# Kernel tuning notes

Hardware: AMD Instinct MI355X
Metric: run time of the kernel (lower is better)

Reference implementation:

```python
import jax, jax.numpy as jnp
import numpy as np

N_NODES = 200000
N_EDGES = 6400000
N_GRAPHS = 2000


def _linear_params(key, fan_in, fan_out):
    k1, k2 = jax.random.split(key)
    bound = 1.0 / np.sqrt(fan_in)
    W = jax.random.uniform(k1, (fan_in, fan_out), minval=-bound, maxval=bound, dtype=jnp.float32)
    b = jax.random.uniform(k2, (fan_out,), minval=-bound, maxval=bound, dtype=jnp.float32)
    return W, b


def setup_inputs() -> dict:
    key = jax.random.key(0)
    ks = jax.random.split(key, 12)
    x = jax.random.normal(ks[0], (N_NODES, 2), dtype=jnp.float32)
    edge_index = jax.random.randint(ks[1], (2, N_EDGES), 0, N_NODES, dtype=jnp.int32)
    batch = jnp.sort(jax.random.randint(ks[2], (N_NODES,), 0, N_GRAPHS, dtype=jnp.int32))
    W1a, b1a = _linear_params(ks[3], 2, 16)
    W1b, b1b = _linear_params(ks[4], 16, 16)
    W2a, b2a = _linear_params(ks[5], 16, 16)
    W2b, b2b = _linear_params(ks[6], 16, 16)
    W3a, b3a = _linear_params(ks[7], 16, 16)
    W3b, b3b = _linear_params(ks[8], 16, 16)
    Wl1, bl1 = _linear_params(ks[9], 16, 16)
    Wl2, bl2 = _linear_params(ks[10], 16, 1)
    return dict(x=x, edge_index=edge_index, batch=batch,
                W1a=W1a, b1a=b1a, W1b=W1b, b1b=b1b,
                W2a=W2a, b2a=b2a, W2b=W2b, b2b=b2b,
                W3a=W3a, b3a=b3a, W3b=W3b, b3b=b3b,
                Wl1=Wl1, bl1=bl1, Wl2=Wl2, bl2=bl2)


def _gin_conv(x, src, dst, Wa, ba, Wb, bb):
    # sum-aggregate neighbor features at destination nodes; eps = 0
    msgs = x[src]                                            # [E, d]
    aggr = jax.ops.segment_sum(msgs, dst, num_segments=N_NODES)  # [N, d]
    h = x + aggr
    h = jax.nn.relu(h @ Wa + ba)
    return h @ Wb + bb


def reference(x, edge_index, batch,
              W1a, b1a, W1b, b1b,
              W2a, b2a, W2b, b2b,
              W3a, b3a, W3b, b3b,
              Wl1, bl1, Wl2, bl2):
    src, dst = edge_index[0], edge_index[1]
    h = jax.nn.relu(_gin_conv(x, src, dst, W1a, b1a, W1b, b1b))
    h = jax.nn.relu(_gin_conv(h, src, dst, W2a, b2a, W2b, b2b))
    h = jax.nn.relu(_gin_conv(h, src, dst, W3a, b3a, W3b, b3b))
    g = jax.ops.segment_sum(h, batch, num_segments=N_GRAPHS)  # global_add_pool -> [G, 16]
    g = jax.nn.relu(g @ Wl1 + bl1)
    return g @ Wl2 + bl2                                      # [G, 1]
```

## Files before the change

### kernel.cpp

```cpp
#include <hip/hip_runtime.h>

#define N_NODES 200000
#define N_EDGES 6400000
#define N_GRAPHS 2000

#define MBSHIFT 11
#define NMB 98
#define MBCAP 67584
#define CHUNK 8192
#define PBLK 782
#define PB 9

#define FSHIFT 7
#define NBUCK 1563
#define CAPF 4608

__device__ __forceinline__ float bf_lo(unsigned v) { return __uint_as_float(v << 16); }
__device__ __forceinline__ float bf_hi(unsigned v) { return __uint_as_float(v & 0xFFFF0000u); }
__device__ __forceinline__ unsigned pack_bf2(float lo, float hi) {
  unsigned a = __float_as_uint(lo), b = __float_as_uint(hi);
  a = (a + 0x7FFFu + ((a >> 16) & 1u)) >> 16;
  b = (b + 0x7FFFu + ((b >> 16) & 1u)) >> 16;
  return a | (b << 16);
}

__global__ __launch_bounds__(256) void init_cursors(int* __restrict__ gcurA,
                                                    int* __restrict__ gcur2) {
  int i = blockIdx.x * 256 + threadIdx.x;
  if (i < NMB) gcurA[i] = i * MBCAP;
  if (i < NMB * 16) gcur2[i] = i * CAPF;
}

__global__ __launch_bounds__(256) void partA(
    const int* __restrict__ src, const int* __restrict__ dst,
    int* __restrict__ gcurA, int* __restrict__ colA) {
  __shared__ int hist[NMB], base[NMB], lcur[NMB];
  __shared__ int sc[128];
  __shared__ int sorted[CHUNK];
  int t = threadIdx.x;
  for (int i = t; i < NMB; i += 256) hist[i] = 0;
  __syncthreads();
  int e0 = blockIdx.x * CHUNK;
  int cnt = N_EDGES - e0; if (cnt > CHUNK) cnt = CHUNK;
  for (int i = t; i < cnt; i += 256) atomicAdd(&hist[dst[e0 + i] >> MBSHIFT], 1);
  __syncthreads();
  if (t < 128) sc[t] = (t < NMB) ? hist[t] : 0;
  __syncthreads();
  for (int off = 1; off < 128; off <<= 1) {
    int v = (t < 128 && t >= off) ? sc[t - off] : 0;
    __syncthreads();
    if (t < 128) sc[t] += v;
    __syncthreads();
  }
  if (t < NMB) {
    lcur[t] = sc[t] - hist[t];
    base[t] = hist[t] ? atomicAdd(&gcurA[t], hist[t]) : 0;
  }
  __syncthreads();
  for (int i = t; i < cnt; i += 256) {
    int d = dst[e0 + i];
    int b = d >> MBSHIFT;
    int r = atomicAdd(&lcur[b], 1);
    sorted[r] = (src[e0 + i] << MBSHIFT) | (d & 2047);
  }
  __syncthreads();
  for (int i = t; i < cnt; i += 256) {
    int lo = 0, hi = NMB;
    while (lo < hi) { int mid = (lo + hi) >> 1; if (sc[mid] <= i) lo = mid + 1; else hi = mid; }
    int b = lo;
    int pos = base[b] + (i - (sc[b] - hist[b]));
    if (pos < (b + 1) * MBCAP) colA[pos] = sorted[i];
  }
}

__global__ __launch_bounds__(256) void partB(
    const int* __restrict__ gcurA, const int* __restrict__ colA,
    int* __restrict__ gcur2, int* __restrict__ col) {
  __shared__ int hist[16], base[16], lcur[16], excl[16], sc16[16];
  __shared__ int sorted[CHUNK];
  int t = threadIdx.x;
  int mb = blockIdx.x / PB, j = blockIdx.x % PB;
  int mbbase = mb * MBCAP;
  int mbcnt = gcurA[mb] - mbbase; if (mbcnt > MBCAP) mbcnt = MBCAP;
  int c0 = j * CHUNK;
  int cnt = mbcnt - c0;
  if (cnt > CHUNK) cnt = CHUNK;
  if (cnt < 0) cnt = 0;
  if (t < 16) hist[t] = 0;
  __syncthreads();
  const int* seg = colA + mbbase + c0;
  for (int i = t; i < cnt; i += 256) atomicAdd(&hist[(seg[i] & 2047) >> FSHIFT], 1);
  __syncthreads();
  if (t == 0) {
    int run = 0;
    for (int b = 0; b < 16; b++) { excl[b] = run; lcur[b] = run; run += hist[b]; sc16[b] = run; }
  }
  if (t < 16) base[t] = hist[t] ? atomicAdd(&gcur2[mb * 16 + t], hist[t]) : 0;
  __syncthreads();
  for (int i = t; i < cnt; i += 256) {
    int p = seg[i];
    int b = (p & 2047) >> FSHIFT;
    int r = atomicAdd(&lcur[b], 1);
    sorted[r] = ((p >> MBSHIFT) << FSHIFT) | (p & 127);
  }
  __syncthreads();
  for (int i = t; i < cnt; i += 256) {
    int lo = 0, hi = 16;
    while (lo < hi) { int mid = (lo + hi) >> 1; if (sc16[mid] <= i) lo = mid + 1; else hi = mid; }
    int b = lo;
    int pos = base[b] + (i - excl[b]);
    if (pos < (mb * 16 + b + 1) * CAPF) col[pos] = sorted[i];
  }
}

__global__ __launch_bounds__(256) void sort_fine(
    const int* __restrict__ gcur2, int* __restrict__ col,
    const float* __restrict__ x,
    int* __restrict__ rowstart, int* __restrict__ rowcnt,
    float* __restrict__ agg2) {
  __shared__ int hist[128], sc[128], lcur[128];
  __shared__ float sagg[256];
  __shared__ int sorted[CAPF];
  int t = threadIdx.x;
  int fb = blockIdx.x;
  int beg = fb * CAPF;
  int cnt = gcur2[fb] - beg; if (cnt > CAPF) cnt = CAPF;
  if (t < 128) hist[t] = 0;
  sagg[t] = 0.f;
  __syncthreads();
  for (int i = t; i < cnt; i += 256) {
    int p = col[beg + i];
    int s = p >> FSHIFT, d = p & 127;
    atomicAdd(&hist[d], 1);
    float2 u = *reinterpret_cast<const float2*>(x + 2 * s);
    atomicAdd(&sagg[d * 2 + 0], u.x);
    atomicAdd(&sagg[d * 2 + 1], u.y);
  }
  __syncthreads();
  if (t < 128) sc[t] = hist[t];
  __syncthreads();
  for (int off = 1; off < 128; off <<= 1) {
    int v = (t < 128 && t >= off) ? sc[t - off] : 0;
    __syncthreads();
    if (t < 128) sc[t] += v;
    __syncthreads();
  }
  if (t < 128) {
    int excl = sc[t] - hist[t];
    lcur[t] = excl;
    int n = fb * 128 + t;
    if (n < N_NODES) { rowstart[n] = beg + excl; rowcnt[n] = hist[t]; }
  }
  {
    int n2 = fb * 256 + t;
    if (n2 < N_NODES * 2) agg2[n2] = sagg[t];
  }
  __syncthreads();
  for (int i = t; i < cnt; i += 256) {
    int p = col[beg + i];
    int r = atomicAdd(&lcur[p & 127], 1);
    sorted[r] = p >> FSHIFT;
  }
  __syncthreads();
  for (int i = t; i < cnt; i += 256) col[beg + i] = sorted[i];
}

__global__ __launch_bounds__(256) void aggr16_wave(
    const int* __restrict__ rowstart, const int* __restrict__ rowcnt,
    const int* __restrict__ col, const uint4* __restrict__ hbf,
    float* __restrict__ agg) {
  int n = blockIdx.x * 4 + (threadIdx.x >> 6);
  int lane = threadIdx.x & 63;
  int e0 = rowstart[n], c = rowcnt[n];
  float a[8];
#pragma unroll
  for (int j = 0; j < 8; j++) a[j] = 0.f;
  int half = lane & 1;
  for (int basei = 0; basei < c; basei += 32) {
    int idx = basei + (lane >> 1);
    if (idx < c) {
      int s = col[e0 + idx];
      uint4 u = hbf[2 * s + half];
      a[0] += bf_lo(u.x); a[1] += bf_hi(u.x);
      a[2] += bf_lo(u.y); a[3] += bf_hi(u.y);
      a[4] += bf_lo(u.z); a[5] += bf_hi(u.z);
      a[6] += bf_lo(u.w); a[7] += bf_hi(u.w);
    }
  }
#pragma unroll
  for (int off = 2; off <= 32; off <<= 1) {
#pragma unroll
    for (int j = 0; j < 8; j++) a[j] += __shfl_xor(a[j], off, 64);
  }
  if (lane < 2) {
    float* dstp = agg + (size_t)n * 16 + 8 * lane;
    *reinterpret_cast<float4*>(dstp)     = make_float4(a[0], a[1], a[2], a[3]);
    *reinterpret_cast<float4*>(dstp + 4) = make_float4(a[4], a[5], a[6], a[7]);
  }
}

__global__ __launch_bounds__(256) void node_l1(
    const float* __restrict__ x, const float* __restrict__ agg2,
    const float* __restrict__ Wa, const float* __restrict__ ba,
    const float* __restrict__ Wb, const float* __restrict__ bb,
    uint4* __restrict__ out) {
  __shared__ float sWa[32], sba[16], sWb[256], sbb[16];
  int t = threadIdx.x;
  if (t < 32) sWa[t] = Wa[t];
  if (t < 16) { sba[t] = ba[t]; sbb[t] = bb[t]; }
  for (int i = t; i < 256; i += 256) sWb[i] = Wb[i];
  __syncthreads();
  int n = blockIdx.x * blockDim.x + t;
  if (n >= N_NODES) return;
  float2 xv = *reinterpret_cast<const float2*>(x + 2 * n);
  float2 av = *reinterpret_cast<const float2*>(agg2 + 2 * n);
  float v0 = xv.x + av.x, v1 = xv.y + av.y;
  float h1[16];
#pragma unroll
  for (int j = 0; j < 16; j++)
    h1[j] = fmaxf(fmaf(v0, sWa[j], fmaf(v1, sWa[16 + j], sba[j])), 0.f);
  float o[16];
#pragma unroll
  for (int j = 0; j < 16; j++) {
    float s = sbb[j];
#pragma unroll
    for (int k = 0; k < 16; k++) s = fmaf(h1[k], sWb[k * 16 + j], s);
    o[j] = fmaxf(s, 0.f);
  }
  out[2 * n]     = make_uint4(pack_bf2(o[0], o[1]),  pack_bf2(o[2], o[3]),
                              pack_bf2(o[4], o[5]),  pack_bf2(o[6], o[7]));
  out[2 * n + 1] = make_uint4(pack_bf2(o[8], o[9]),  pack_bf2(o[10], o[11]),
                              pack_bf2(o[12], o[13]), pack_bf2(o[14], o[15]));
}

__global__ __launch_bounds__(256) void node16(
    const uint4* __restrict__ hin, const float* __restrict__ aggr,
    const float* __restrict__ Wa, const float* __restrict__ ba,
    const float* __restrict__ Wb, const float* __restrict__ bb,
    uint4* __restrict__ out) {
  __shared__ float sWa[256], sba[16], sWb[256], sbb[16];
  int t = threadIdx.x;
  if (t < 16) { sba[t] = ba[t]; sbb[t] = bb[t]; }
  for (int i = t; i < 256; i += 256) { sWa[i] = Wa[i]; sWb[i] = Wb[i]; }
  __syncthreads();
  int n = blockIdx.x * blockDim.x + t;
  if (n >= N_NODES) return;
  uint4 r0 = hin[2 * n], r1 = hin[2 * n + 1];
  const float4* ap = reinterpret_cast<const float4*>(aggr + 16 * n);
  float4 a0 = ap[0], a1 = ap[1], a2 = ap[2], a3 = ap[3];
  float v[16];
  v[0]  = bf_lo(r0.x) + a0.x;  v[1]  = bf_hi(r0.x) + a0.y;
  v[2]  = bf_lo(r0.y) + a0.z;  v[3]  = bf_hi(r0.y) + a0.w;
  v[4]  = bf_lo(r0.z) + a1.x;  v[5]  = bf_hi(r0.z) + a1.y;
  v[6]  = bf_lo(r0.w) + a1.z;  v[7]  = bf_hi(r0.w) + a1.w;
  v[8]  = bf_lo(r1.x) + a2.x;  v[9]  = bf_hi(r1.x) + a2.y;
  v[10] = bf_lo(r1.y) + a2.z;  v[11] = bf_hi(r1.y) + a2.w;
  v[12] = bf_lo(r1.z) + a3.x;  v[13] = bf_hi(r1.z) + a3.y;
  v[14] = bf_lo(r1.w) + a3.z;  v[15] = bf_hi(r1.w) + a3.w;
  float h1[16];
#pragma unroll
  for (int j = 0; j < 16; j++) {
    float s = sba[j];
#pragma unroll
    for (int k = 0; k < 16; k++) s = fmaf(v[k], sWa[k * 16 + j], s);
    h1[j] = fmaxf(s, 0.f);
  }
  float o[16];
#pragma unroll
  for (int j = 0; j < 16; j++) {
    float s = sbb[j];
#pragma unroll
    for (int k = 0; k < 16; k++) s = fmaf(h1[k], sWb[k * 16 + j], s);
    o[j] = fmaxf(s, 0.f);
  }
  out[2 * n]     = make_uint4(pack_bf2(o[0], o[1]),  pack_bf2(o[2], o[3]),
                              pack_bf2(o[4], o[5]),  pack_bf2(o[6], o[7]));
  out[2 * n + 1] = make_uint4(pack_bf2(o[8], o[9]),  pack_bf2(o[10], o[11]),
                              pack_bf2(o[12], o[13]), pack_bf2(o[14], o[15]));
}

__global__ __launch_bounds__(64) void pool_kernel(
    const uint4* __restrict__ h, const int* __restrict__ batch,
    float* __restrict__ g) {
  int gr = blockIdx.x;
  int lo = 0, hi = N_NODES;
  while (lo < hi) { int mid = (lo + hi) >> 1; if (batch[mid] < gr) lo = mid + 1; else hi = mid; }
  int start = lo;
  hi = N_NODES;
  while (lo < hi) { int mid = (lo + hi) >> 1; if (batch[mid] < gr + 1) lo = mid + 1; else hi = mid; }
  int end = lo;
  float acc[16];
#pragma unroll
  for (int j = 0; j < 16; j++) acc[j] = 0.f;
  for (int n = start + threadIdx.x; n < end; n += 64) {
    uint4 r0 = h[2 * n], r1 = h[2 * n + 1];
    acc[0]  += bf_lo(r0.x); acc[1]  += bf_hi(r0.x);
    acc[2]  += bf_lo(r0.y); acc[3]  += bf_hi(r0.y);
    acc[4]  += bf_lo(r0.z); acc[5]  += bf_hi(r0.z);
    acc[6]  += bf_lo(r0.w); acc[7]  += bf_hi(r0.w);
    acc[8]  += bf_lo(r1.x); acc[9]  += bf_hi(r1.x);
    acc[10] += bf_lo(r1.y); acc[11] += bf_hi(r1.y);
    acc[12] += bf_lo(r1.z); acc[13] += bf_hi(r1.z);
    acc[14] += bf_lo(r1.w); acc[15] += bf_hi(r1.w);
  }
#pragma unroll
  for (int j = 0; j < 16; j++) {
#pragma unroll
    for (int off = 32; off > 0; off >>= 1) acc[j] += __shfl_xor(acc[j], off, 64);
  }
  if (threadIdx.x == 0) {
    float4* gp = reinterpret_cast<float4*>(g + gr * 16);
#pragma unroll
    for (int q = 0; q < 4; q++)
      gp[q] = make_float4(acc[4 * q], acc[4 * q + 1], acc[4 * q + 2], acc[4 * q + 3]);
  }
}

__global__ __launch_bounds__(256) void head_kernel(
    const float* __restrict__ g,
    const float* __restrict__ Wl1, const float* __restrict__ bl1,
    const float* __restrict__ Wl2, const float* __restrict__ bl2,
    float* __restrict__ out) {
  __shared__ float sW1[256], sb1[16], sW2[16];
  int t = threadIdx.x;
  if (t < 16) { sb1[t] = bl1[t]; sW2[t] = Wl2[t]; }
  for (int i = t; i < 256; i += 256) sW1[i] = Wl1[i];
  __syncthreads();
  int gr = blockIdx.x * blockDim.x + t;
  if (gr >= N_GRAPHS) return;
  float v[16];
  const float4* gp = reinterpret_cast<const float4*>(g + 16 * gr);
#pragma unroll
  for (int q = 0; q < 4; q++) {
    float4 gv = gp[q];
    v[4 * q + 0] = gv.x; v[4 * q + 1] = gv.y; v[4 * q + 2] = gv.z; v[4 * q + 3] = gv.w;
  }
  float o = bl2[0];
#pragma unroll
  for (int j = 0; j < 16; j++) {
    float s = sb1[j];
#pragma unroll
    for (int k = 0; k < 16; k++) s = fmaf(v[k], sW1[k * 16 + j], s);
    o = fmaf(fmaxf(s, 0.f), sW2[j], o);
  }
  out[gr] = o;
}

extern "C" void kernel_launch(void* const* d_in, const int* in_sizes, int n_in,
                              void* d_out, int out_size, void* d_ws, size_t ws_size,
                              hipStream_t stream) {
  const float* x     = (const float*)d_in[0];
  const int*   ei    = (const int*)d_in[1];
  const int*   src   = ei;
  const int*   dst   = ei + N_EDGES;
  const int*   batch = (const int*)d_in[2];
  const float* W1a = (const float*)d_in[3];  const float* b1a = (const float*)d_in[4];
  const float* W1b = (const float*)d_in[5];  const float* b1b = (const float*)d_in[6];
  const float* W2a = (const float*)d_in[7];  const float* b2a = (const float*)d_in[8];
  const float* W2b = (const float*)d_in[9];  const float* b2b = (const float*)d_in[10];
  const float* W3a = (const float*)d_in[11]; const float* b3a = (const float*)d_in[12];
  const float* W3b = (const float*)d_in[13]; const float* b3b = (const float*)d_in[14];
  const float* Wl1 = (const float*)d_in[15]; const float* bl1 = (const float*)d_in[16];
  const float* Wl2 = (const float*)d_in[17]; const float* bl2 = (const float*)d_in[18];
  float* out = (float*)d_out;

  int*   gcurA    = (int*)d_ws;
  int*   gcur2    = gcurA + 128;
  int*   rowstart = gcur2 + 2048;
  int*   rowcnt   = rowstart + 200192;
  float* agg2     = (float*)(rowcnt + 200192);
  int*   col      = (int*)agg2 + 400384;
  int*   U        = col + (size_t)NBUCK * CAPF;
  int*   colA     = U;
  float* agg      = (float*)U;
  uint4* hA       = (uint4*)(agg + (size_t)N_NODES * 16);
  uint4* hB       = hA + (size_t)N_NODES * 2;
  float* g        = (float*)(hB + (size_t)N_NODES * 2);

  const int NWAVE_BLK = N_NODES / 4;
  dim3 ngrid((N_NODES + 255) / 256);

  init_cursors<<<(NMB * 16 + 255) / 256, 256, 0, stream>>>(gcurA, gcur2);
  partA<<<PBLK, 256, 0, stream>>>(src, dst, gcurA, colA);
  partB<<<NMB * PB, 256, 0, stream>>>(gcurA, colA, gcur2, col);
  sort_fine<<<NBUCK, 256, 0, stream>>>(gcur2, col, x, rowstart, rowcnt, agg2);

  node_l1<<<ngrid, 256, 0, stream>>>(x, agg2, W1a, b1a, W1b, b1b, hA);
  aggr16_wave<<<NWAVE_BLK, 256, 0, stream>>>(rowstart, rowcnt, col, hA, agg);
  node16<<<ngrid, 256, 0, stream>>>(hA, agg, W2a, b2a, W2b, b2b, hB);
  aggr16_wave<<<NWAVE_BLK, 256, 0, stream>>>(rowstart, rowcnt, col, hB, agg);
  node16<<<ngrid, 256, 0, stream>>>(hB, agg, W3a, b3a, W3b, b3b, hA);

  pool_kernel<<<N_GRAPHS, 64, 0, stream>>>(hA, batch, g);
  head_kernel<<<(N_GRAPHS + 255) / 256, 256, 0, stream>>>(g, Wl1, bl1, Wl2, bl2, out);
}
```

Before: 404.7 us.

## Split layer-1 aggregation out of sort_fine into CSR gather kernel, halve partA chunk

Moves the 2-wide first-layer neighbor sum out of sort_fine, where it used shared-memory float atomics, into a new aggr2_wave kernel that gathers over the finished CSR rows with 32 lanes per node and shuffle reductions. It also halves partA's chunk size, doubling its block count and cutting its shared memory per block, and simplifies the aggr16 loop bounds. This trades LDS atomic contention in sort_fine for an extra kernel launch and a second pass over col. Float summation order also changes.

```diff
diff --git a/kernel.cpp b/kernel.cpp
--- a/kernel.cpp
+++ b/kernel.cpp
@@ -7,8 +7,9 @@
 #define MBSHIFT 11
 #define NMB 98
 #define MBCAP 67584
-#define CHUNK 8192
-#define PBLK 782
+#define CHUNKA 4096
+#define PBLKA 1563
+#define CHUNKB 8192
 #define PB 9
 
 #define FSHIFT 7
@@ -36,12 +37,12 @@
     int* __restrict__ gcurA, int* __restrict__ colA) {
   __shared__ int hist[NMB], base[NMB], lcur[NMB];
   __shared__ int sc[128];
-  __shared__ int sorted[CHUNK];
+  __shared__ int sorted[CHUNKA];
   int t = threadIdx.x;
   for (int i = t; i < NMB; i += 256) hist[i] = 0;
   __syncthreads();
-  int e0 = blockIdx.x * CHUNK;
-  int cnt = N_EDGES - e0; if (cnt > CHUNK) cnt = CHUNK;
+  int e0 = blockIdx.x * CHUNKA;
+  int cnt = N_EDGES - e0; if (cnt > CHUNKA) cnt = CHUNKA;
   for (int i = t; i < cnt; i += 256) atomicAdd(&hist[dst[e0 + i] >> MBSHIFT], 1);
   __syncthreads();
   if (t < 128) sc[t] = (t < NMB) ? hist[t] : 0;
@@ -77,14 +78,14 @@
     const int* __restrict__ gcurA, const int* __restrict__ colA,
     int* __restrict__ gcur2, int* __restrict__ col) {
   __shared__ int hist[16], base[16], lcur[16], excl[16], sc16[16];
-  __shared__ int sorted[CHUNK];
+  __shared__ int sorted[CHUNKB];
   int t = threadIdx.x;
   int mb = blockIdx.x / PB, j = blockIdx.x % PB;
   int mbbase = mb * MBCAP;
   int mbcnt = gcurA[mb] - mbbase; if (mbcnt > MBCAP) mbcnt = MBCAP;
-  int c0 = j * CHUNK;
+  int c0 = j * CHUNKB;
   int cnt = mbcnt - c0;
-  if (cnt > CHUNK) cnt = CHUNK;
+  if (cnt > CHUNKB) cnt = CHUNKB;
   if (cnt < 0) cnt = 0;
   if (t < 16) hist[t] = 0;
   __syncthreads();
@@ -115,27 +116,16 @@
 
 __global__ __launch_bounds__(256) void sort_fine(
     const int* __restrict__ gcur2, int* __restrict__ col,
-    const float* __restrict__ x,
-    int* __restrict__ rowstart, int* __restrict__ rowcnt,
-    float* __restrict__ agg2) {
+    int* __restrict__ rowstart, int* __restrict__ rowcnt) {
   __shared__ int hist[128], sc[128], lcur[128];
-  __shared__ float sagg[256];
   __shared__ int sorted[CAPF];
   int t = threadIdx.x;
   int fb = blockIdx.x;
   int beg = fb * CAPF;
   int cnt = gcur2[fb] - beg; if (cnt > CAPF) cnt = CAPF;
   if (t < 128) hist[t] = 0;
-  sagg[t] = 0.f;
-  __syncthreads();
-  for (int i = t; i < cnt; i += 256) {
-    int p = col[beg + i];
-    int s = p >> FSHIFT, d = p & 127;
-    atomicAdd(&hist[d], 1);
-    float2 u = *reinterpret_cast<const float2*>(x + 2 * s);
-    atomicAdd(&sagg[d * 2 + 0], u.x);
-    atomicAdd(&sagg[d * 2 + 1], u.y);
-  }
+  __syncthreads();
+  for (int i = t; i < cnt; i += 256) atomicAdd(&hist[col[beg + i] & 127], 1);
   __syncthreads();
   if (t < 128) sc[t] = hist[t];
   __syncthreads();
@@ -151,10 +141,6 @@
     int n = fb * 128 + t;
     if (n < N_NODES) { rowstart[n] = beg + excl; rowcnt[n] = hist[t]; }
   }
-  {
-    int n2 = fb * 256 + t;
-    if (n2 < N_NODES * 2) agg2[n2] = sagg[t];
-  }
   __syncthreads();
   for (int i = t; i < cnt; i += 256) {
     int p = col[beg + i];
@@ -163,6 +149,29 @@
   }
   __syncthreads();
   for (int i = t; i < cnt; i += 256) col[beg + i] = sorted[i];
+}
+
+__global__ __launch_bounds__(256) void aggr2_wave(
+    const int* __restrict__ rowstart, const int* __restrict__ rowcnt,
+    const int* __restrict__ col, const float* __restrict__ x,
+    float* __restrict__ agg2) {
+  int n = blockIdx.x * 8 + (threadIdx.x >> 5);
+  int l32 = threadIdx.x & 31;
+  int e0 = rowstart[n], c = rowcnt[n];
+  float a0 = 0.f, a1 = 0.f;
+  for (int idx = l32; idx < c; idx += 32) {
+    int s = col[e0 + idx];
+    float2 u = *reinterpret_cast<const float2*>(x + 2 * s);
+    a0 += u.x; a1 += u.y;
+  }
+#pragma unroll
+  for (int off = 1; off <= 16; off <<= 1) {
+    a0 += __shfl_xor(a0, off, 64);
+    a1 += __shfl_xor(a1, off, 64);
+  }
+  if (l32 == 0) {
+    *reinterpret_cast<float2*>(agg2 + 2 * n) = make_float2(a0, a1);
+  }
 }
 
 __global__ __launch_bounds__(256) void aggr16_wave(
@@ -176,16 +185,13 @@
 #pragma unroll
   for (int j = 0; j < 8; j++) a[j] = 0.f;
   int half = lane & 1;
-  for (int basei = 0; basei < c; basei += 32) {
-    int idx = basei + (lane >> 1);
-    if (idx < c) {
-      int s = col[e0 + idx];
-      uint4 u = hbf[2 * s + half];
-      a[0] += bf_lo(u.x); a[1] += bf_hi(u.x);
-      a[2] += bf_lo(u.y); a[3] += bf_hi(u.y);
-      a[4] += bf_lo(u.z); a[5] += bf_hi(u.z);
-      a[6] += bf_lo(u.w); a[7] += bf_hi(u.w);
-    }
+  for (int idx = (lane >> 1); idx < c; idx += 32) {
+    int s = col[e0 + idx];
+    uint4 u = hbf[2 * s + half];
+    a[0] += bf_lo(u.x); a[1] += bf_hi(u.x);
+    a[2] += bf_lo(u.y); a[3] += bf_hi(u.y);
+    a[4] += bf_lo(u.z); a[5] += bf_hi(u.z);
+    a[6] += bf_lo(u.w); a[7] += bf_hi(u.w);
   }
 #pragma unroll
   for (int off = 2; off <= 32; off <<= 1) {
@@ -378,13 +384,15 @@
   float* g        = (float*)(hB + (size_t)N_NODES * 2);
 
   const int NWAVE_BLK = N_NODES / 4;
+  const int N2_BLK = N_NODES / 8;
   dim3 ngrid((N_NODES + 255) / 256);
 
   init_cursors<<<(NMB * 16 + 255) / 256, 256, 0, stream>>>(gcurA, gcur2);
-  partA<<<PBLK, 256, 0, stream>>>(src, dst, gcurA, colA);
+  partA<<<PBLKA, 256, 0, stream>>>(src, dst, gcurA, colA);
   partB<<<NMB * PB, 256, 0, stream>>>(gcurA, colA, gcur2, col);
-  sort_fine<<<NBUCK, 256, 0, stream>>>(gcur2, col, x, rowstart, rowcnt, agg2);
-
+  sort_fine<<<NBUCK, 256, 0, stream>>>(gcur2, col, rowstart, rowcnt);
+
+  aggr2_wave<<<N2_BLK, 256, 0, stream>>>(rowstart, rowcnt, col, x, agg2);
   node_l1<<<ngrid, 256, 0, stream>>>(x, agg2, W1a, b1a, W1b, b1b, hA);
   aggr16_wave<<<NWAVE_BLK, 256, 0, stream>>>(rowstart, rowcnt, col, hA, agg);
   node16<<<ngrid, 256, 0, stream>>>(hA, agg, W2a, b2a, W2b, b2b, hB);
```

After: 365.5 us. -9.7%, faster.
